# Kernel optimization log

Measured on AMD Instinct MI355X. Metric: run time of the kernel, lower is better.

The kernel has to match this reference:

```python
import jax, jax.numpy as jnp
import numpy as np

T, B, E, H = 2048, 2, 2048, 16
D = E // H  # 128


def setup_inputs() -> dict:
    key = jax.random.key(0)
    ks = jax.random.split(key, 4)
    query = jax.random.normal(ks[0], (T, B, E), dtype=jnp.float32)
    Wqkv = jax.random.normal(ks[1], (3 * E, E), dtype=jnp.float32) * 0.02
    bqkv = jnp.zeros((3 * E,), dtype=jnp.float32)
    Wo = jax.random.normal(ks[2], (E, E), dtype=jnp.float32) * 0.02
    bo = jnp.zeros((E,), dtype=jnp.float32)
    # Llama rotary frequencies: freqs_cis[t, j] = exp(i * t * theta^{-2j/D})
    inv_freq = 1.0 / (10000.0 ** (np.arange(0, D, 2, dtype=np.float32) / D))  # (D/2,)
    angles = np.arange(T, dtype=np.float32)[:, None] * inv_freq[None, :]       # (T, D/2)
    freqs_cos = jnp.asarray(np.cos(angles), dtype=jnp.float32)
    freqs_sin = jnp.asarray(np.sin(angles), dtype=jnp.float32)
    return {"query": query, "Wqkv": Wqkv, "bqkv": bqkv, "Wo": Wo, "bo": bo,
            "freqs_cos": freqs_cos, "freqs_sin": freqs_sin}


def _apply_rope(x, cos, sin):
    # Faithful to metaseq: x is (T, B, E) but view()-ed as (B, T, H, D);
    # jnp.reshape is the same row-major reinterpretation as torch .view().
    xr = x.reshape(B, T, H, D // 2, 2)
    x0, x1 = xr[..., 0], xr[..., 1]
    c = cos[None, :, None, :]  # broadcast over batch and heads, seq_dim=1
    s = sin[None, :, None, :]
    o0 = x0 * c - x1 * s
    o1 = x0 * s + x1 * c
    return jnp.stack([o0, o1], axis=-1).reshape(T, B, E)


def reference(query, Wqkv, bqkv, Wo, bo, freqs_cos, freqs_sin):
    # Combined QKV projection (ColumnParallelLinear, world_size=1), split order (k, v, q)
    kvq = jnp.einsum('tbe,fe->tbf', query, Wqkv) + bqkv  # (T, B, 3E)
    k, v, q = jnp.split(kvq, 3, axis=-1)
    q = _apply_rope(q, freqs_cos, freqs_sin)
    k = _apply_rope(k, freqs_cos, freqs_sin)
    # scaling split as sqrt(head_dim^-0.5) on both q and k (baddbmm path)
    s = jnp.asarray(D, jnp.float32) ** -0.25
    qb = q.reshape(T, B * H, D).swapaxes(0, 1) * s   # (BH, T, D)
    kb = k.reshape(T, B * H, D).swapaxes(0, 1) * s   # (BH, S, D)
    vb = v.reshape(T, B * H, D).swapaxes(0, 1)       # (BH, S, D)
    scores = jnp.einsum('btd,bsd->bts', qb, kb)      # (BH, T, S)
    causal = jnp.tril(jnp.ones((T, T), dtype=bool))  # ScaledUpperTriangMaskedSoftmax
    scores = jnp.where(causal[None, :, :], scores, jnp.finfo(scores.dtype).min)
    probs = jax.nn.softmax(scores, axis=-1)          # dropout p=0 -> identity
    attn = jnp.einsum('bts,bsd->btd', probs, vb)     # (BH, T, D)
    attn = attn.swapaxes(0, 1).reshape(T, B, E)
    # RowParallelLinear with skip_bias_add=True: bias returned separately (not added)
    out = jnp.einsum('tbe,fe->tbf', attn, Wo)
    return out
```

## Files before the change

### kernel.cpp

```cpp
#include <hip/hip_runtime.h>
#include <stdint.h>

typedef unsigned short u16;
typedef __attribute__((ext_vector_type(4))) float f32x4;
typedef __attribute__((ext_vector_type(8))) short bf16x8;
typedef __attribute__((ext_vector_type(8))) u16 u16x8;

#define T_SEQ  2048
#define EMB    2048
#define HD     128
#define NHEAD  16
#define NTOK   4096
#define NE3    6144
#define SCALE  0.29730177875068026f
#define LOG2E  1.44269504088896f

typedef __attribute__((address_space(3))) char* lds_t;
typedef const __attribute__((address_space(1))) char* gl_t;

__device__ __forceinline__ void gld16(const void* g, void* l) {
  __builtin_amdgcn_global_load_lds((gl_t)g, (lds_t)l, 16, 0, 0);
}

__device__ __forceinline__ u16 f2bf(float f) {
  union { float f; uint32_t u; } c; c.f = f;
  uint32_t r = c.u + 0x7fffu + ((c.u >> 16) & 1u);
  return (u16)(r >> 16);
}

__global__ __launch_bounds__(256) void cvt_bf16(const float* __restrict__ in,
                                                u16* __restrict__ out, int n8) {
  int i = blockIdx.x * 256 + threadIdx.x;
  if (i >= n8) return;
  const float4* p = (const float4*)in + (size_t)i * 2;
  float4 a = p[0], b = p[1];
  u16x8 o;
  o[0]=f2bf(a.x); o[1]=f2bf(a.y); o[2]=f2bf(a.z); o[3]=f2bf(a.w);
  o[4]=f2bf(b.x); o[5]=f2bf(b.y); o[6]=f2bf(b.z); o[7]=f2bf(b.w);
  *((u16x8*)out + i) = o;
}


__device__ __forceinline__ bf16x8 rdfrag(const char* slot, int row, int lq) {
  return *(const bf16x8*)(slot + row*64 + ((lq ^ ((row >> 1) & 3)) << 4));
}
__device__ __forceinline__ void stg(const char* g, int K2, int kb,
                                    char* slot, int j, int tid) {
  int lb = j*4096 + tid*16;
  int row = lb >> 6, c = (lb >> 4) & 3;
  gld16(g + (size_t)row*K2 + kb + ((c ^ ((row >> 1) & 3)) << 4), slot + lb);
}

template<int EPI, int NBN>
__global__ __launch_bounds__(256, 2) void gemmW(
    const u16* __restrict__ A, const u16* __restrict__ Bm, int K, int N,
    const float* __restrict__ cosT, const float* __restrict__ sinT,
    const float* __restrict__ bias,
    u16* __restrict__ Qh, u16* __restrict__ Kh, u16* __restrict__ Vt,
    float* __restrict__ Cout)
{
  __shared__ __align__(16) char lds[73728];
  const int tid = threadIdx.x;
  const int lane = tid & 63, wn = tid >> 6;
  const int l15 = lane & 15, lq = lane >> 4;

  const int i = blockIdx.x;
  const int r = i >> 8, x = i & 7, s = (i >> 3) & 31;
  const int regionId = r*8 + x;
  const int RM = regionId & 3, RN = regionId >> 2;
  const int bM = RM*8 + (s >> 2);
  const int bN = RN*4 + (s & 3);

  const char* Ag = (const char*)(A + (size_t)bM * 128 * K);
  const char* Bg = (const char*)(Bm + (size_t)bN * 256 * K);
  const int K2 = K * 2;
  const int nQ = K >> 5;

  #pragma unroll
  for (int q = 0; q < 2; ++q) {
    stg(Ag, K2, q*64, lds + q*8192, 0, tid);
    stg(Ag, K2, q*64, lds + q*8192, 1, tid);
    stg(Bg, K2, q*64, lds + 24576 + q*16384, 0, tid);
    stg(Bg, K2, q*64, lds + 24576 + q*16384, 1, tid);
    stg(Bg, K2, q*64, lds + 24576 + q*16384, 2, tid);
    stg(Bg, K2, q*64, lds + 24576 + q*16384, 3, tid);
  }

  f32x4 acc[8][4] = {};
  int sRd = 0, sWr = 2;

  for (int q = 0; q < nQ; ++q) {
    const int qs = q + 2 < nQ ? q + 2 : nQ - 1;
    const char* Asl = lds + sRd*8192;
    const char* Bsl = lds + 24576 + sRd*16384;
    char* AslS = lds + sWr*8192;
    char* BslS = lds + 24576 + sWr*16384;

    asm volatile("s_waitcnt vmcnt(6)" ::: "memory");
    __builtin_amdgcn_s_barrier();
    __builtin_amdgcn_sched_barrier(0);

    bf16x8 af[8], bf[4];
    #pragma unroll
    for (int j = 0; j < 8; j++) af[j] = rdfrag(Asl, j*16 + l15, lq);
    #pragma unroll
    for (int j = 0; j < 4; j++) bf[j] = rdfrag(Bsl, wn*64 + j*16 + l15, lq);
    stg(Ag, K2, qs*64, AslS, 0, tid);
    stg(Ag, K2, qs*64, AslS, 1, tid);
    stg(Bg, K2, qs*64, BslS, 0, tid);
    stg(Bg, K2, qs*64, BslS, 1, tid);
    stg(Bg, K2, qs*64, BslS, 2, tid);
    stg(Bg, K2, qs*64, BslS, 3, tid);
    asm volatile("s_waitcnt lgkmcnt(0)" ::: "memory");
    __builtin_amdgcn_sched_barrier(0);
    __builtin_amdgcn_s_setprio(1);
    #pragma unroll
    for (int mi = 0; mi < 8; mi++)
      #pragma unroll
      for (int ni = 0; ni < 4; ni++)
        acc[mi][ni] = __builtin_amdgcn_mfma_f32_16x16x32_bf16(af[mi], bf[ni], acc[mi][ni], 0, 0, 0);
    __builtin_amdgcn_s_setprio(0);

    sRd = sRd + 1 < 3 ? sRd + 1 : 0;
    sWr = sWr + 1 < 3 ? sWr + 1 : 0;
  }
  asm volatile("s_waitcnt vmcnt(0)" ::: "memory");

  if (EPI == 0) {
    #pragma unroll
    for (int mi = 0; mi < 8; mi++) {
      int row = bM*128 + mi*16 + lq*4;
      #pragma unroll
      for (int ni = 0; ni < 4; ni++) {
        int col = bN*256 + wn*64 + ni*16 + l15;
        #pragma unroll
        for (int rr = 0; rr < 4; rr++)
          Cout[(size_t)(row + rr) * N + col] = acc[mi][ni][rr];
      }
    }
  } else {
    const int cbase = bN*256 + wn*64;
    const int seg  = cbase >> 11;
    const int head = (cbase >> 7) & 15;
    #pragma unroll
    for (int mi = 0; mi < 8; mi++) {
      #pragma unroll
      for (int ni = 0; ni < 4; ni++) {
        int col = cbase + ni*16 + l15;
        int d = col & 127;
        float bi = bias[col];
        f32x4 v = acc[mi][ni];
        #pragma unroll
        for (int rr = 0; rr < 4; rr++) {
          int n = bM*128 + mi*16 + lq*4 + rr;
          float val = v[rr] + bi;
          int t = n >> 1, b = n & 1;
          int bh = b*NHEAD + head;
          if (seg == 1) {
            Vt[((size_t)bh*HD + d)*T_SEQ + t] = f2bf(val);
          } else {
            float par = __shfl_xor(val, 1);
            int fidx = d >> 1;
            float cs = cosT[(n & (T_SEQ-1))*64 + fidx];
            float sn = sinT[(n & (T_SEQ-1))*64 + fidx];
            val = (d & 1) ? (par*sn + val*cs) : (val*cs - par*sn);
            val *= SCALE;
            u16* dst = (seg == 0) ? Kh : Qh;
            dst[((size_t)bh*T_SEQ + t)*HD + d] = f2bf(val);
          }
        }
      }
    }
  }
}

__global__ __launch_bounds__(256, 4) void attn_fwd(
    const u16* __restrict__ Qh, const u16* __restrict__ Kh,
    const u16* __restrict__ Vt, u16* __restrict__ O)
{
  const int i = blockIdx.x;
  const int kk = i >> 8, c = i & 255;
  const int bh = (c >> 5) + kk * 8;
  const int b5 = c & 31;
  const int qb = (kk & 1) ? (31 - b5) : b5;

  const int tid = threadIdx.x, lane = tid & 63, w = tid >> 6;
  const int l15 = lane & 15, lq = lane >> 4;

  __shared__ u16 Ks[64*128];
  __shared__ u16 Vs[128*64];
  __shared__ char Ps[4][2048];

  const int q0 = qb*64 + w*16;
  bf16x8 qf[4];
  #pragma unroll
  for (int dc = 0; dc < 4; dc++)
    qf[dc] = *(const bf16x8*)(Qh + ((size_t)bh*T_SEQ + q0 + l15)*HD + dc*32 + lq*8);

  f32x4 o[8] = {};
  float m[4], l_[4];
  #pragma unroll
  for (int r = 0; r < 4; r++) { m[r] = -1e30f; l_[r] = 0.f; }

  const int nkb = qb + 1;
  for (int kb = 0; kb < nkb; ++kb) {
    #pragma unroll
    for (int j = 0; j < 4; j++) {
      int lb = tid*16 + j*4096;
      int row = lb >> 8, bir = lb & 255;
      int sb = bir ^ ((row & 7) << 4);
      gld16((const char*)Kh + (((size_t)bh*T_SEQ + kb*64 + row) << 8) + sb,
            (char*)Ks + lb);
    }
    #pragma unroll
    for (int j = 0; j < 4; j++) {
      int lb = tid*16 + j*4096;
      int row = lb >> 7, bir = lb & 127;
      int sb = bir ^ ((row & 7) << 4);
      gld16((const char*)Vt + ((size_t)(bh*HD + row)*T_SEQ)*2 + kb*128 + sb,
            (char*)Vs + lb);
    }
    __syncthreads();

    f32x4 sacc[4];
    #pragma unroll
    for (int nf = 0; nf < 4; nf++) {
      f32x4 z = {};
      sacc[nf] = z;
      #pragma unroll
      for (int dc = 0; dc < 4; dc++) {
        int row = nf*16 + l15;
        int bir = (dc*64 + lq*16) ^ ((row & 7) << 4);
        bf16x8 kf = *(const bf16x8*)((const char*)Ks + row*256 + bir);
        sacc[nf] = __builtin_amdgcn_mfma_f32_16x16x32_bf16(qf[dc], kf, sacc[nf], 0, 0, 0);
      }
    }

    if (kb == qb) {
      #pragma unroll
      for (int nf = 0; nf < 4; nf++)
        #pragma unroll
        for (int r = 0; r < 4; r++) {
          int key = kb*64 + nf*16 + l15;
          int qr  = q0 + lq*4 + r;
          if (key > qr) sacc[nf][r] = -1e30f;
        }
    }

    #pragma unroll
    for (int r = 0; r < 4; r++) {
      float mx = fmaxf(fmaxf(sacc[0][r], sacc[1][r]), fmaxf(sacc[2][r], sacc[3][r]));
      mx = fmaxf(mx, __shfl_xor(mx, 1));
      mx = fmaxf(mx, __shfl_xor(mx, 2));
      mx = fmaxf(mx, __shfl_xor(mx, 4));
      mx = fmaxf(mx, __shfl_xor(mx, 8));
      float newm = fmaxf(m[r], mx);
      float scale = exp2f((m[r] - newm) * LOG2E);
      float sum = 0.f;
      #pragma unroll
      for (int nf = 0; nf < 4; nf++) {
        float p = exp2f((sacc[nf][r] - newm) * LOG2E);
        sacc[nf][r] = p;
        sum += p;
      }
      sum += __shfl_xor(sum, 1);
      sum += __shfl_xor(sum, 2);
      sum += __shfl_xor(sum, 4);
      sum += __shfl_xor(sum, 8);
      l_[r] = l_[r] * scale + sum;
      m[r] = newm;
      #pragma unroll
      for (int nf = 0; nf < 8; nf++) o[nf][r] *= scale;
    }

    #pragma unroll
    for (int nf = 0; nf < 4; nf++)
      #pragma unroll
      for (int r = 0; r < 4; r++) {
        int prow = lq*4 + r;
        int pbyte = prow*128 + ((((nf*16 + l15)*2)) ^ ((prow & 7) << 4));
        *(u16*)(Ps[w] + pbyte) = f2bf(sacc[nf][r]);
      }

    #pragma unroll
    for (int kc = 0; kc < 2; kc++) {
      int pb = (kc*64 + lq*16) ^ ((l15 & 7) << 4);
      bf16x8 pf = *(const bf16x8*)(Ps[w] + l15*128 + pb);
      #pragma unroll
      for (int nf = 0; nf < 8; nf++) {
        int row = nf*16 + l15;
        int bir = (kc*64 + lq*16) ^ ((row & 7) << 4);
        bf16x8 vf = *(const bf16x8*)((const char*)Vs + row*128 + bir);
        o[nf] = __builtin_amdgcn_mfma_f32_16x16x32_bf16(pf, vf, o[nf], 0, 0, 0);
      }
    }
    __syncthreads();
  }

  const int b = bh >> 4, h = bh & 15;
  #pragma unroll
  for (int r = 0; r < 4; r++) {
    float inv = 1.0f / l_[r];
    int t = q0 + lq*4 + r;
    size_t base = ((size_t)(t*2 + b))*EMB + h*HD;
    #pragma unroll
    for (int nf = 0; nf < 8; nf++)
      O[base + nf*16 + l15] = f2bf(o[nf][r] * inv);
  }
}

extern "C" void kernel_launch(void* const* d_in, const int* in_sizes, int n_in,
                              void* d_out, int out_size, void* d_ws, size_t ws_size,
                              hipStream_t stream) {
  const float* query = (const float*)d_in[0];
  const float* Wqkv  = (const float*)d_in[1];
  const float* bqkv  = (const float*)d_in[2];
  const float* Wo    = (const float*)d_in[3];
  const float* fcos  = (const float*)d_in[5];
  const float* fsin  = (const float*)d_in[6];
  float* out = (float*)d_out;
  char* ws = (char*)d_ws;

  u16* WQb = (u16*)(ws + 0);
  u16* WOb = (u16*)(ws + 25165824);
  u16* A1  = (u16*)(ws + 33554432);
  u16* QH  = (u16*)(ws + 50331648);
  u16* KH  = (u16*)(ws + 67108864);
  u16* VT  = (u16*)(ws + 83886080);

  cvt_bf16<<<4096, 256, 0, stream>>>(query, A1, 1048576);
  cvt_bf16<<<6144, 256, 0, stream>>>(Wqkv, WQb, 1572864);
  cvt_bf16<<<2048, 256, 0, stream>>>(Wo,   WOb,  524288);

  gemmW<1, 24><<<768, 256, 0, stream>>>(A1, WQb, 2048, NE3,
                                        fcos, fsin, bqkv, QH, KH, VT, nullptr);

  attn_fwd<<<1024, 256, 0, stream>>>(QH, KH, VT, A1);

  gemmW<0, 8><<<256, 256, 0, stream>>>(A1, WOb, 2048, EMB,
                                       nullptr, nullptr, nullptr,
                                       nullptr, nullptr, nullptr, out);
}
```

Baseline: 345.6 us.

## Enlarge GEMM tiles to 256x256 with 8 waves and double-buffered 128-wide K stages

Replaces the 128x256-tile, 4-wave, 3-slot pipelined GEMM with a 256x256-tile, 8-wave kernel whose LDS is double-buffered over 128-deep K chunks, each split into two 64-deep sub-steps. This raises arithmetic intensity per tile and halves global reloads of the B operand. The cost is 128KB of LDS per block, which limits occupancy to one block per CU despite the launch bound of two, and the QKV GEMM and output GEMM now launch only 384 and 128 blocks on 256 CUs, so some CUs sit idle and the last wave is poorly balanced.

```diff
diff --git a/kernel.cpp b/kernel.cpp
--- a/kernel.cpp
+++ b/kernel.cpp
@@ -44,92 +44,87 @@
 __device__ __forceinline__ bf16x8 rdfrag(const char* slot, int row, int lq) {
   return *(const bf16x8*)(slot + row*64 + ((lq ^ ((row >> 1) & 3)) << 4));
 }
-__device__ __forceinline__ void stg(const char* g, int K2, int kb,
-                                    char* slot, int j, int tid) {
-  int lb = j*4096 + tid*16;
+__device__ __forceinline__ void stg512(const char* g, int K2, int kbyte,
+                                       char* slot, int j, int tid) {
+  int lb = j*8192 + tid*16;
   int row = lb >> 6, c = (lb >> 4) & 3;
-  gld16(g + (size_t)row*K2 + kb + ((c ^ ((row >> 1) & 3)) << 4), slot + lb);
-}
-
-template<int EPI, int NBN>
-__global__ __launch_bounds__(256, 2) void gemmW(
+  gld16(g + (size_t)row*K2 + kbyte + ((c ^ ((row >> 1) & 3)) << 4), slot + lb);
+}
+
+template<int EPI>
+__global__ __launch_bounds__(512, 2) void gemm256(
     const u16* __restrict__ A, const u16* __restrict__ Bm, int K, int N,
     const float* __restrict__ cosT, const float* __restrict__ sinT,
     const float* __restrict__ bias,
     u16* __restrict__ Qh, u16* __restrict__ Kh, u16* __restrict__ Vt,
     float* __restrict__ Cout)
 {
-  __shared__ __align__(16) char lds[73728];
+  __shared__ __align__(16) char lds[131072];
   const int tid = threadIdx.x;
-  const int lane = tid & 63, wn = tid >> 6;
+  const int lane = tid & 63, w = tid >> 6;
+  const int wm = w >> 2, wn = w & 3;
   const int l15 = lane & 15, lq = lane >> 4;
 
   const int i = blockIdx.x;
-  const int r = i >> 8, x = i & 7, s = (i >> 3) & 31;
-  const int regionId = r*8 + x;
-  const int RM = regionId & 3, RN = regionId >> 2;
-  const int bM = RM*8 + (s >> 2);
-  const int bN = RN*4 + (s & 3);
-
-  const char* Ag = (const char*)(A + (size_t)bM * 128 * K);
+  const int regionId = i >> 4, s = i & 15;
+  const int bM = (regionId & 3)*4 + (s >> 2);
+  const int bN = (regionId >> 2)*4 + (s & 3);
+
+  const char* Ag = (const char*)(A + (size_t)bM * 256 * K);
   const char* Bg = (const char*)(Bm + (size_t)bN * 256 * K);
   const int K2 = K * 2;
-  const int nQ = K >> 5;
-
-  #pragma unroll
-  for (int q = 0; q < 2; ++q) {
-    stg(Ag, K2, q*64, lds + q*8192, 0, tid);
-    stg(Ag, K2, q*64, lds + q*8192, 1, tid);
-    stg(Bg, K2, q*64, lds + 24576 + q*16384, 0, tid);
-    stg(Bg, K2, q*64, lds + 24576 + q*16384, 1, tid);
-    stg(Bg, K2, q*64, lds + 24576 + q*16384, 2, tid);
-    stg(Bg, K2, q*64, lds + 24576 + q*16384, 3, tid);
-  }
+  const int nT = K >> 6;
+
+  stg512(Ag, K2, 0,  lds + 0,     0, tid);  stg512(Ag, K2, 0,  lds + 0,     1, tid);
+  stg512(Bg, K2, 0,  lds + 32768, 0, tid);  stg512(Bg, K2, 0,  lds + 32768, 1, tid);
+  stg512(Ag, K2, 64, lds + 16384, 0, tid);  stg512(Ag, K2, 64, lds + 16384, 1, tid);
+  stg512(Bg, K2, 64, lds + 49152, 0, tid);  stg512(Bg, K2, 64, lds + 49152, 1, tid);
 
   f32x4 acc[8][4] = {};
-  int sRd = 0, sWr = 2;
-
-  for (int q = 0; q < nQ; ++q) {
-    const int qs = q + 2 < nQ ? q + 2 : nQ - 1;
-    const char* Asl = lds + sRd*8192;
-    const char* Bsl = lds + 24576 + sRd*16384;
-    char* AslS = lds + sWr*8192;
-    char* BslS = lds + 24576 + sWr*16384;
-
-    asm volatile("s_waitcnt vmcnt(6)" ::: "memory");
-    __builtin_amdgcn_s_barrier();
-    __builtin_amdgcn_sched_barrier(0);
-
-    bf16x8 af[8], bf[4];
-    #pragma unroll
-    for (int j = 0; j < 8; j++) af[j] = rdfrag(Asl, j*16 + l15, lq);
-    #pragma unroll
-    for (int j = 0; j < 4; j++) bf[j] = rdfrag(Bsl, wn*64 + j*16 + l15, lq);
-    stg(Ag, K2, qs*64, AslS, 0, tid);
-    stg(Ag, K2, qs*64, AslS, 1, tid);
-    stg(Bg, K2, qs*64, BslS, 0, tid);
-    stg(Bg, K2, qs*64, BslS, 1, tid);
-    stg(Bg, K2, qs*64, BslS, 2, tid);
-    stg(Bg, K2, qs*64, BslS, 3, tid);
-    asm volatile("s_waitcnt lgkmcnt(0)" ::: "memory");
-    __builtin_amdgcn_sched_barrier(0);
-    __builtin_amdgcn_s_setprio(1);
-    #pragma unroll
-    for (int mi = 0; mi < 8; mi++)
-      #pragma unroll
-      for (int ni = 0; ni < 4; ni++)
-        acc[mi][ni] = __builtin_amdgcn_mfma_f32_16x16x32_bf16(af[mi], bf[ni], acc[mi][ni], 0, 0, 0);
-    __builtin_amdgcn_s_setprio(0);
-
-    sRd = sRd + 1 < 3 ? sRd + 1 : 0;
-    sWr = sWr + 1 < 3 ? sWr + 1 : 0;
+
+  for (int t = 0; t < nT; ++t) {
+    const int b = t & 1;
+    const char* Ab = lds + b*65536;
+    const char* Bb = lds + b*65536 + 32768;
+    char* Abn = lds + (b^1)*65536;
+    char* Bbn = lds + (b^1)*65536 + 32768;
+    const int tn = (t + 1 < nT) ? t + 1 : t;
+
+    #pragma unroll
+    for (int ks = 0; ks < 2; ++ks) {
+      asm volatile("s_waitcnt vmcnt(4)" ::: "memory");
+      __builtin_amdgcn_s_barrier();
+      __builtin_amdgcn_sched_barrier(0);
+
+      const char* As = Ab + ks*16384;
+      const char* Bs = Bb + ks*16384;
+      bf16x8 af[8], bf[4];
+      #pragma unroll
+      for (int j = 0; j < 8; j++) af[j] = rdfrag(As, wm*128 + j*16 + l15, lq);
+      #pragma unroll
+      for (int j = 0; j < 4; j++) bf[j] = rdfrag(Bs, wn*64 + j*16 + l15, lq);
+      const int kb = tn*128 + ks*64;
+      stg512(Ag, K2, kb, Abn + ks*16384, 0, tid);
+      stg512(Ag, K2, kb, Abn + ks*16384, 1, tid);
+      stg512(Bg, K2, kb, Bbn + ks*16384, 0, tid);
+      stg512(Bg, K2, kb, Bbn + ks*16384, 1, tid);
+      asm volatile("s_waitcnt lgkmcnt(0)" ::: "memory");
+      __builtin_amdgcn_sched_barrier(0);
+      __builtin_amdgcn_s_setprio(1);
+      #pragma unroll
+      for (int mi = 0; mi < 8; mi++)
+        #pragma unroll
+        for (int ni = 0; ni < 4; ni++)
+          acc[mi][ni] = __builtin_amdgcn_mfma_f32_16x16x32_bf16(af[mi], bf[ni], acc[mi][ni], 0, 0, 0);
+      __builtin_amdgcn_s_setprio(0);
+    }
   }
   asm volatile("s_waitcnt vmcnt(0)" ::: "memory");
 
   if (EPI == 0) {
     #pragma unroll
     for (int mi = 0; mi < 8; mi++) {
-      int row = bM*128 + mi*16 + lq*4;
+      int row = bM*256 + wm*128 + mi*16 + lq*4;
       #pragma unroll
       for (int ni = 0; ni < 4; ni++) {
         int col = bN*256 + wn*64 + ni*16 + l15;
@@ -152,7 +147,7 @@
         f32x4 v = acc[mi][ni];
         #pragma unroll
         for (int rr = 0; rr < 4; rr++) {
-          int n = bM*128 + mi*16 + lq*4 + rr;
+          int n = bM*256 + wm*128 + mi*16 + lq*4 + rr;
           float val = v[rr] + bi;
           int t = n >> 1, b = n & 1;
           int bh = b*NHEAD + head;
@@ -332,12 +327,12 @@
   cvt_bf16<<<6144, 256, 0, stream>>>(Wqkv, WQb, 1572864);
   cvt_bf16<<<2048, 256, 0, stream>>>(Wo,   WOb,  524288);
 
-  gemmW<1, 24><<<768, 256, 0, stream>>>(A1, WQb, 2048, NE3,
-                                        fcos, fsin, bqkv, QH, KH, VT, nullptr);
+  gemm256<1><<<384, 512, 0, stream>>>(A1, WQb, 2048, NE3,
+                                      fcos, fsin, bqkv, QH, KH, VT, nullptr);
 
   attn_fwd<<<1024, 256, 0, stream>>>(QH, KH, VT, A1);
 
-  gemmW<0, 8><<<256, 256, 0, stream>>>(A1, WOb, 2048, EMB,
-                                       nullptr, nullptr, nullptr,
-                                       nullptr, nullptr, nullptr, out);
-}
+  gemm256<0><<<128, 512, 0, stream>>>(A1, WOb, 2048, EMB,
+                                      nullptr, nullptr, nullptr,
+                                      nullptr, nullptr, nullptr, out);
+}
```

Result: slower. 365.3 us (+5.7%).
